# Kernel optimization log

Measured on AMD Instinct MI355X. Metric: run time of the kernel, lower is better.

## Reference

```python
import jax, jax.numpy as jnp
import numpy as np

N_NODES = 100000
N_USERS = 60000
N_MOVIES = 40000
N_EDGES = 1200000
D_IN = 64
D_EMB = 64


def setup_inputs() -> dict:
    key = jax.random.key(0)
    ks = jax.random.split(key, 6)
    x = jax.random.normal(ks[0], (N_NODES, D_IN), dtype=jnp.float32)
    edge_index = jax.random.randint(ks[1], (2, N_EDGES), 0, N_NODES, dtype=jnp.int64)
    # Glorot-ish init for the two GCNConv linear weights
    W1 = jax.random.normal(ks[2], (D_IN, D_EMB), dtype=jnp.float32) * (1.0 / np.sqrt(D_IN))
    b1 = jnp.zeros((D_EMB,), dtype=jnp.float32)
    W2 = jax.random.normal(ks[3], (D_EMB, D_EMB), dtype=jnp.float32) * (1.0 / np.sqrt(D_EMB))
    b2 = jnp.zeros((D_EMB,), dtype=jnp.float32)
    return {"x": x, "edge_index": edge_index, "W1": W1, "b1": b1, "W2": W2, "b2": b2}


def gcn_conv(x, W, b, src, dst):
    """PyG GCNConv: D^{-1/2}(A+I)D^{-1/2} X W + b with symmetric norm and self-loops."""
    h = x @ W  # [N, D_out]
    ones = jnp.ones(src.shape[0], dtype=h.dtype)
    # degree includes self-loop (+1)
    deg = jax.ops.segment_sum(ones, dst, num_segments=N_NODES) + 1.0
    dinv = jax.lax.rsqrt(deg)  # [N]
    coef = dinv[src] * dinv[dst]  # [E]
    agg = jax.ops.segment_sum(h[src] * coef[:, None], dst, num_segments=N_NODES)
    # self-loop contribution: norm = dinv[i]^2
    return agg + h * (dinv * dinv)[:, None] + b


def reference(x, edge_index, W1, b1, W2, b2):
    src, dst = edge_index[0], edge_index[1]
    h = gcn_conv(x, W1, b1, src, dst)
    h = jax.nn.relu(h)  # dropout is identity in eval mode
    h = gcn_conv(h, W2, b2, src, dst)
    user = h[:N_USERS]
    movie = h[N_USERS:N_USERS + N_MOVIES]
    return user, movie, h
```

## Files before the change

kernel.cpp:

```cpp
#include <hip/hip_runtime.h>

#define NN 100000
#define NE 1200000
#define DD 64
#define SCH 1024
#define SNB ((NN + SCH - 1) / SCH)

#define KCH3 96
#define CEH3 (NE / KCH3)
#define P3 4
#define BINS3 (NN / P3)
#define BINW3 (BINS3 / 4)
#define KSEG 4
#define KPS (KCH3 / KSEG)
#define NW4 (NN / 4)
#define HISTB (KCH3 * P3)
#define GEMMB ((NN + 255) / 256)

static __device__ __forceinline__ unsigned short f2bf(float f) {
    unsigned int u = __float_as_uint(f);
    u += 0x7fffu + ((u >> 16) & 1u);
    return (unsigned short)(u >> 16);
}
static __device__ __forceinline__ float bf_lo(unsigned int u) { return __uint_as_float(u << 16); }
static __device__ __forceinline__ float bf_hi(unsigned int u) { return __uint_as_float(u & 0xffff0000u); }

__global__ __launch_bounds__(1024) void k_histgemm(const int* __restrict__ dst,
                                                   unsigned char* __restrict__ H,
                                                   unsigned char* __restrict__ rank8,
                                                   const float* __restrict__ X,
                                                   const float* __restrict__ W,
                                                   unsigned short* __restrict__ Hb) {
    __shared__ union SM {
        unsigned int bins[BINW3];
        struct { float4 Ws4[64][16]; float Xs[64][68]; } g;
    } sm;
    int t = threadIdx.x;
    if (blockIdx.x < HISTB) {
        int k = blockIdx.x >> 2;
        int p = blockIdx.x & 3;
        for (int i = t; i < BINW3; i += 1024) sm.bins[i] = 0u;
        __syncthreads();
        int lo = p * BINS3;
        int beg = k * CEH3;
        for (int e4 = beg + t * 4; e4 < beg + CEH3; e4 += 4096) {
            int4 d4 = *(const int4*)&dst[e4];
            int dd[4] = {d4.x, d4.y, d4.z, d4.w};
#pragma unroll
            for (int j = 0; j < 4; ++j) {
                unsigned int r = (unsigned int)(dd[j] - lo);
                if (r < (unsigned int)BINS3) {
                    unsigned int sh = (r & 3u) << 3;
                    unsigned int old = atomicAdd(&sm.bins[r >> 2], 1u << sh);
                    rank8[e4 + j] = (unsigned char)((old >> sh) & 0xffu);
                }
            }
        }
        __syncthreads();
        unsigned int* Hw = (unsigned int*)(H + (size_t)k * NN + lo);
        for (int i = t; i < BINW3; i += 1024) Hw[i] = sm.bins[i];
    } else {
        const float4* W4 = (const float4*)W;
        sm.g.Ws4[t >> 4][t & 15] = W4[t];
        int row0 = (int)(blockIdx.x - HISTB) * 256;
        const float4* X4 = (const float4*)X;
        int r = t >> 4, q = t & 15;
#pragma unroll
        for (int s = 0; s < 4; ++s) {
            int row = row0 + s * 64 + r;
            float4 v = make_float4(0.f, 0.f, 0.f, 0.f);
            if (row < NN) v = X4[row * 16 + q];
            __syncthreads();
            *((float4*)&sm.g.Xs[r][q * 4]) = v;
            __syncthreads();
            float4 acc = make_float4(0.f, 0.f, 0.f, 0.f);
#pragma unroll 4
            for (int k = 0; k < 64; ++k) {
                float4 w = sm.g.Ws4[k][q];
                float x = sm.g.Xs[r][k];
                acc.x += x * w.x; acc.y += x * w.y; acc.z += x * w.z; acc.w += x * w.w;
            }
            if (row < NN) {
                ushort4 o;
                o.x = f2bf(acc.x); o.y = f2bf(acc.y); o.z = f2bf(acc.z); o.w = f2bf(acc.w);
                *((ushort4*)&Hb[(size_t)row * 64 + q * 4]) = o;
            }
        }
    }
}

__global__ __launch_bounds__(256) void k_cseg_sum(const unsigned int* __restrict__ H32,
                                                  unsigned int* __restrict__ aux) {
    int wd = blockIdx.x * 256 + threadIdx.x;
    int seg = blockIdx.y;
    if (wd >= NW4) return;
    unsigned int s = 0;
#pragma unroll
    for (int k = 0; k < KPS; ++k)
        s += H32[(size_t)(seg * KPS + k) * NW4 + wd];
    aux[seg * NW4 + wd] = s;
}

__global__ __launch_bounds__(256) void k_cseg_scan2(unsigned int* __restrict__ H32,
                                                    const unsigned int* __restrict__ aux,
                                                    int* __restrict__ rowptr,
                                                    int* __restrict__ part,
                                                    float* __restrict__ dinv) {
    __shared__ int wsum[4];
    int t = threadIdx.x;
    int wd = blockIdx.x * 256 + t;
    int seg = blockIdx.y;
    bool valid = wd < NW4;
    unsigned int s = 0;
    if (valid) {
        unsigned int base = 0;
        for (int i = 0; i < seg; ++i) base += aux[i * NW4 + wd];
        s = base;
#pragma unroll
        for (int k = 0; k < KPS; ++k) {
            size_t idx = (size_t)(seg * KPS + k) * NW4 + wd;
            unsigned int v = H32[idx];
            H32[idx] = s;
            s += v;
        }
    }
    if (seg != KSEG - 1) return;
    int d0 = valid ? (int)(s & 0xffu) : 0;
    int d1 = valid ? (int)((s >> 8) & 0xffu) : 0;
    int d2 = valid ? (int)((s >> 16) & 0xffu) : 0;
    int d3 = valid ? (int)(s >> 24) : 0;
    int idx = blockIdx.x * SCH + t * 4;
    if (valid) {
        float4 dv;
        dv.x = rsqrtf((float)d0 + 1.0f);
        dv.y = rsqrtf((float)d1 + 1.0f);
        dv.z = rsqrtf((float)d2 + 1.0f);
        dv.w = rsqrtf((float)d3 + 1.0f);
        *(float4*)&dinv[idx] = dv;
    }
    int ssum = d0 + d1 + d2 + d3;
    int lane = t & 63;
    int incl = ssum;
#pragma unroll
    for (int off = 1; off < 64; off <<= 1) {
        int v = __shfl_up(incl, off);
        if (lane >= off) incl += v;
    }
    int wv = t >> 6;
    if (lane == 63) wsum[wv] = incl;
    __syncthreads();
    int woff = 0;
#pragma unroll
    for (int i = 0; i < 4; ++i) if (i < wv) woff += wsum[i];
    int excl = woff + incl - ssum;
    if (valid) {
        int4 rp = make_int4(excl, excl + d0, excl + d0 + d1, excl + d0 + d1 + d2);
        *(int4*)&rowptr[idx] = rp;
    }
    if (t == 255) part[blockIdx.x] = woff + incl;
}

__global__ __launch_bounds__(128) void k_scan_part(int* __restrict__ part, int* __restrict__ rowptr) {
    __shared__ int sm[128];
    int t = threadIdx.x;
    int v = (t < SNB) ? part[t] : 0;
    sm[t] = v;
    __syncthreads();
    for (int off = 1; off < 128; off <<= 1) {
        int add = (t >= off) ? sm[t - off] : 0;
        __syncthreads();
        sm[t] += add;
        __syncthreads();
    }
    if (t == SNB - 1) rowptr[NN] = v;
    if (t < SNB) part[t] = sm[t] - v;
}

__global__ __launch_bounds__(256) void k_fill4(const int* __restrict__ src,
                                               const int* __restrict__ dst,
                                               const unsigned char* __restrict__ rank8,
                                               const unsigned char* __restrict__ H,
                                               const int* __restrict__ rowptr,
                                               const int* __restrict__ part,
                                               const float* __restrict__ dinv,
                                               int2* __restrict__ cc) {
    int e4 = (blockIdx.x * 256 + threadIdx.x) * 4;
    if (e4 >= NE) return;
    int4 d4 = *(const int4*)&dst[e4];
    int4 s4 = *(const int4*)&src[e4];
    unsigned int r4 = *(const unsigned int*)&rank8[e4];
    int dd[4] = {d4.x, d4.y, d4.z, d4.w};
    int ss[4] = {s4.x, s4.y, s4.z, s4.w};
    int k = e4 / CEH3;
#pragma unroll
    for (int j = 0; j < 4; ++j) {
        int d = dd[j], s = ss[j];
        int base = rowptr[d] + part[d >> 10] + (int)H[(size_t)k * NN + d];
        int pos = base + (int)((r4 >> (8 * j)) & 0xffu);
        cc[pos] = make_int2(s, __float_as_int(dinv[s] * dinv[d]));
    }
}

__global__ void k_hist_rank(const int* __restrict__ dst, int* __restrict__ degi,
                            int* __restrict__ rank, int ne) {
    int i = blockIdx.x * blockDim.x + threadIdx.x;
    if (i < ne) rank[i] = atomicAdd(&degi[dst[i]], 1);
}

__global__ __launch_bounds__(256) void k_scan_local(const int* __restrict__ degi,
                                                    int* __restrict__ rowptr,
                                                    int* __restrict__ part,
                                                    float* __restrict__ dinv) {
    __shared__ int wsum[4];
    int t = threadIdx.x;
    int idx = blockIdx.x * SCH + t * 4;
    int d0 = 0, d1 = 0, d2 = 0, d3 = 0;
    if (idx + 3 < NN) {
        int4 v = *(const int4*)&degi[idx];
        d0 = v.x; d1 = v.y; d2 = v.z; d3 = v.w;
        float4 dv;
        dv.x = rsqrtf((float)d0 + 1.0f);
        dv.y = rsqrtf((float)d1 + 1.0f);
        dv.z = rsqrtf((float)d2 + 1.0f);
        dv.w = rsqrtf((float)d3 + 1.0f);
        *(float4*)&dinv[idx] = dv;
    } else {
        if (idx     < NN) { d0 = degi[idx];     dinv[idx]     = rsqrtf((float)d0 + 1.0f); }
        if (idx + 1 < NN) { d1 = degi[idx + 1]; dinv[idx + 1] = rsqrtf((float)d1 + 1.0f); }
        if (idx + 2 < NN) { d2 = degi[idx + 2]; dinv[idx + 2] = rsqrtf((float)d2 + 1.0f); }
        if (idx + 3 < NN) { d3 = degi[idx + 3]; dinv[idx + 3] = rsqrtf((float)d3 + 1.0f); }
    }
    int s = d0 + d1 + d2 + d3;
    int lane = t & 63;
    int incl = s;
#pragma unroll
    for (int off = 1; off < 64; off <<= 1) {
        int v = __shfl_up(incl, off);
        if (lane >= off) incl += v;
    }
    int wv = t >> 6;
    if (lane == 63) wsum[wv] = incl;
    __syncthreads();
    int woff = 0;
#pragma unroll
    for (int i = 0; i < 4; ++i) if (i < wv) woff += wsum[i];
    int excl = woff + incl - s;
    if (idx     < NN) rowptr[idx]     = excl;
    if (idx + 1 < NN) rowptr[idx + 1] = excl + d0;
    if (idx + 2 < NN) rowptr[idx + 2] = excl + d0 + d1;
    if (idx + 3 < NN) rowptr[idx + 3] = excl + d0 + d1 + d2;
    if (t == 255) part[blockIdx.x] = woff + incl;
}

__global__ void k_scan_add(int* __restrict__ rowptr, const int* __restrict__ part) {
    int i = blockIdx.x * blockDim.x + threadIdx.x;
    if (i < NN) rowptr[i] += part[i >> 10];
    if (i == 0) rowptr[NN] = NE;
}

__global__ void k_fill_rank(const int* __restrict__ src, const int* __restrict__ dst,
                            const int* __restrict__ rank, const int* __restrict__ rowptr,
                            int* __restrict__ csr_src, int ne) {
    int e = blockIdx.x * blockDim.x + threadIdx.x;
    if (e < ne) csr_src[rowptr[dst[e]] + rank[e]] = src[e];
}

__global__ __launch_bounds__(256) void k_pack(const int* __restrict__ rowptr,
                                              const int* __restrict__ csr,
                                              const float* __restrict__ dinv,
                                              int2* __restrict__ cc) {
    int n = blockIdx.x * 256 + threadIdx.x;
    if (n >= NN) return;
    float dn = dinv[n];
    for (int e = rowptr[n]; e < rowptr[n + 1]; ++e) {
        int s = csr[e];
        cc[e] = make_int2(s, __float_as_int(dinv[s] * dn));
    }
}

__global__ __launch_bounds__(256) void k_gemm_bf(const float* __restrict__ X,
                                                 const float* __restrict__ W,
                                                 unsigned short* __restrict__ Hb,
                                                 int nrows) {
    __shared__ float4 Ws4[64][16];
    __shared__ float  Xs[64][68];
    int tid = threadIdx.x;
    const float4* W4 = (const float4*)W;
    for (int i = tid; i < 64 * 16; i += 256) Ws4[i >> 4][i & 15] = W4[i];
    int row0 = blockIdx.x * 64;
    const float4* X4 = (const float4*)X;
    for (int i = tid; i < 64 * 16; i += 256) {
        int r = i >> 4, q = i & 15;
        int row = row0 + r;
        float4 v = make_float4(0.f, 0.f, 0.f, 0.f);
        if (row < nrows) v = X4[row * 16 + q];
        *((float4*)&Xs[r][q * 4]) = v;
    }
    __syncthreads();
    int c4 = tid & 15;
    int rg = tid >> 4;
    float4 acc0 = make_float4(0.f, 0.f, 0.f, 0.f);
    float4 acc1 = acc0, acc2 = acc0, acc3 = acc0;
#pragma unroll 4
    for (int k = 0; k < 64; ++k) {
        float4 w = Ws4[k][c4];
        float x0 = Xs[rg * 4 + 0][k];
        float x1 = Xs[rg * 4 + 1][k];
        float x2 = Xs[rg * 4 + 2][k];
        float x3 = Xs[rg * 4 + 3][k];
        acc0.x += x0 * w.x; acc0.y += x0 * w.y; acc0.z += x0 * w.z; acc0.w += x0 * w.w;
        acc1.x += x1 * w.x; acc1.y += x1 * w.y; acc1.z += x1 * w.z; acc1.w += x1 * w.w;
        acc2.x += x2 * w.x; acc2.y += x2 * w.y; acc2.z += x2 * w.z; acc2.w += x2 * w.w;
        acc3.x += x3 * w.x; acc3.y += x3 * w.y; acc3.z += x3 * w.z; acc3.w += x3 * w.w;
    }
    float4 accs[4] = {acc0, acc1, acc2, acc3};
#pragma unroll
    for (int i = 0; i < 4; ++i) {
        int row = row0 + rg * 4 + i;
        if (row < nrows) {
            ushort4 o;
            o.x = f2bf(accs[i].x); o.y = f2bf(accs[i].y);
            o.z = f2bf(accs[i].z); o.w = f2bf(accs[i].w);
            *((ushort4*)&Hb[row * 64 + c4 * 4]) = o;
        }
    }
}

static __device__ __forceinline__ void gather8(const unsigned short* __restrict__ Hb,
                                               const int2* __restrict__ cc,
                                               int e0, int deg, int dmax, int cg,
                                               float acc[8]) {
#define LDE(T, S, C) { bool _v = (T) < deg; int2 _w = _v ? cc[e0 + (T)] : make_int2(0, 0); \
                       S = _w.x; C = __int_as_float(_w.y); }
#define GAT(U, S) U = *(const uint4*)(Hb + (size_t)(S) * 64 + cg * 8);
#define CONS(U, C) { acc[0] += bf_lo(U.x) * (C);  acc[1] += bf_hi(U.x) * (C); \
                     acc[2] += bf_lo(U.y) * (C);  acc[3] += bf_hi(U.y) * (C); \
                     acc[4] += bf_lo(U.z) * (C);  acc[5] += bf_hi(U.z) * (C); \
                     acc[6] += bf_lo(U.w) * (C);  acc[7] += bf_hi(U.w) * (C); }
    int s0, s1, s2, s3; float c0, c1, c2, c3;
    LDE(0, s0, c0); LDE(1, s1, c1); LDE(2, s2, c2); LDE(3, s3, c3);
    uint4 u0, u1, u2, u3;
    GAT(u0, s0); GAT(u1, s1); GAT(u2, s2); GAT(u3, s3);
    for (int t = 0; t < dmax; t += 4) {
        int sn0, sn1, sn2, sn3; float cn0, cn1, cn2, cn3;
        LDE(t + 4, sn0, cn0); LDE(t + 5, sn1, cn1);
        LDE(t + 6, sn2, cn2); LDE(t + 7, sn3, cn3);
        CONS(u0, c0); GAT(u0, sn0); c0 = cn0;
        CONS(u1, c1); GAT(u1, sn1); c1 = cn1;
        CONS(u2, c2); GAT(u2, sn2); c2 = cn2;
        CONS(u3, c3); GAT(u3, sn3); c3 = cn3;
    }
#undef LDE
#undef GAT
#undef CONS
}

__global__ __launch_bounds__(256) void k_reduce_g2(const unsigned short* __restrict__ Hb,
                                                   const int* __restrict__ rowptr,
                                                   const int* __restrict__ part,
                                                   const int2* __restrict__ cc,
                                                   const float* __restrict__ dinv,
                                                   const float* __restrict__ bias,
                                                   const float* __restrict__ W2,
                                                   unsigned short* __restrict__ Hb2) {
    __shared__ float4 Ws4[64][16];
    __shared__ float rows[32][68];
    int t = threadIdx.x;
    const float4* W4 = (const float4*)W2;
    for (int i = t; i < 1024; i += 256) Ws4[i >> 4][i & 15] = W4[i];

    int n = blockIdx.x * 32 + (t >> 3);
    int cg = t & 7;
    bool nv = n < NN;
    float din = nv ? dinv[n] : 0.f;
    uint4 us = make_uint4(0u, 0u, 0u, 0u);
    int e0 = 0, deg = 0;
    if (nv) {
        us = *(const uint4*)(Hb + (size_t)n * 64 + cg * 8);
        int rp0 = rowptr[n] + part[n >> 10];
        int rp1 = rowptr[n + 1] + part[(n + 1) >> 10];
        e0 = rp0; deg = rp1 - rp0;
    }
    int dmax = deg;
    dmax = max(dmax, __shfl_xor(dmax, 8));
    dmax = max(dmax, __shfl_xor(dmax, 16));
    dmax = max(dmax, __shfl_xor(dmax, 32));

    float acc[8];
#pragma unroll
    for (int j = 0; j < 8; ++j) acc[j] = 0.f;
    gather8(Hb, cc, e0, deg, dmax, cg, acc);

    float ddn = din * din;
    float4 b0 = *(const float4*)(bias + cg * 8);
    float4 b1 = *(const float4*)(bias + cg * 8 + 4);
    float4 o0, o1;
    o0.x = fmaxf(acc[0] + bf_lo(us.x) * ddn + b0.x, 0.f);
    o0.y = fmaxf(acc[1] + bf_hi(us.x) * ddn + b0.y, 0.f);
    o0.z = fmaxf(acc[2] + bf_lo(us.y) * ddn + b0.z, 0.f);
    o0.w = fmaxf(acc[3] + bf_hi(us.y) * ddn + b0.w, 0.f);
    o1.x = fmaxf(acc[4] + bf_lo(us.z) * ddn + b1.x, 0.f);
    o1.y = fmaxf(acc[5] + bf_hi(us.z) * ddn + b1.y, 0.f);
    o1.z = fmaxf(acc[6] + bf_lo(us.w) * ddn + b1.z, 0.f);
    o1.w = fmaxf(acc[7] + bf_hi(us.w) * ddn + b1.w, 0.f);
    int node = t >> 3;
    *(float4*)&rows[node][cg * 8]     = o0;
    *(float4*)&rows[node][cg * 8 + 4] = o1;
    __syncthreads();

    int c2 = t & 7;
    float a0 = 0.f, a1 = 0.f, a2 = 0.f, a3 = 0.f, a4 = 0.f, a5 = 0.f, a6 = 0.f, a7 = 0.f;
#pragma unroll 4
    for (int k = 0; k < 64; ++k) {
        float r = rows[node][k];
        float4 w0 = Ws4[k][c2 * 2];
        float4 w1 = Ws4[k][c2 * 2 + 1];
        a0 += r * w0.x; a1 += r * w0.y; a2 += r * w0.z; a3 += r * w0.w;
        a4 += r * w1.x; a5 += r * w1.y; a6 += r * w1.z; a7 += r * w1.w;
    }
    if (nv) {
        uint4 pk;
        pk.x = (unsigned int)f2bf(a0) | ((unsigned int)f2bf(a1) << 16);
        pk.y = (unsigned int)f2bf(a2) | ((unsigned int)f2bf(a3) << 16);
        pk.z = (unsigned int)f2bf(a4) | ((unsigned int)f2bf(a5) << 16);
        pk.w = (unsigned int)f2bf(a6) | ((unsigned int)f2bf(a7) << 16);
        *(uint4*)&Hb2[(size_t)n * 64 + c2 * 8] = pk;
    }
}

__global__ __launch_bounds__(256) void k_reduce2(const unsigned short* __restrict__ Hb,
                                                 const int* __restrict__ rowptr,
                                                 const int* __restrict__ part,
                                                 const int2* __restrict__ cc,
                                                 const float* __restrict__ dinv,
                                                 const float* __restrict__ bias,
                                                 float* __restrict__ out0,
                                                 float* __restrict__ out1) {
    int n = blockIdx.x * 32 + (threadIdx.x >> 3);
    if (n >= NN) return;
    int cg = threadIdx.x & 7;
    float din = dinv[n];
    uint4 us = *(const uint4*)(Hb + (size_t)n * 64 + cg * 8);
    int rp0 = rowptr[n] + part[n >> 10];
    int rp1 = rowptr[n + 1] + part[(n + 1) >> 10];
    int e0 = rp0, deg = rp1 - rp0;
    int dmax = deg;
    dmax = max(dmax, __shfl_xor(dmax, 8));
    dmax = max(dmax, __shfl_xor(dmax, 16));
    dmax = max(dmax, __shfl_xor(dmax, 32));

    float acc[8];
#pragma unroll
    for (int j = 0; j < 8; ++j) acc[j] = 0.f;
    gather8(Hb, cc, e0, deg, dmax, cg, acc);

    float ddn = din * din;
    float4 b0 = *(const float4*)(bias + cg * 8);
    float4 b1 = *(const float4*)(bias + cg * 8 + 4);
    float4 o0, o1;
    o0.x = acc[0] + bf_lo(us.x) * ddn + b0.x;
    o0.y = acc[1] + bf_hi(us.x) * ddn + b0.y;
    o0.z = acc[2] + bf_lo(us.y) * ddn + b0.z;
    o0.w = acc[3] + bf_hi(us.y) * ddn + b0.w;
    o1.x = acc[4] + bf_lo(us.z) * ddn + b1.x;
    o1.y = acc[5] + bf_hi(us.z) * ddn + b1.y;
    o1.z = acc[6] + bf_lo(us.w) * ddn + b1.z;
    o1.w = acc[7] + bf_hi(us.w) * ddn + b1.w;
    *(float4*)(out0 + (size_t)n * 64 + cg * 8)     = o0;
    *(float4*)(out0 + (size_t)n * 64 + cg * 8 + 4) = o1;
    *(float4*)(out1 + (size_t)n * 64 + cg * 8)     = o0;
    *(float4*)(out1 + (size_t)n * 64 + cg * 8 + 4) = o1;
}

extern "C" void kernel_launch(void* const* d_in, const int* in_sizes, int n_in,
                              void* d_out, int out_size, void* d_ws, size_t ws_size,
                              hipStream_t stream) {
    const float* x  = (const float*)d_in[0];
    const int*   ei = (const int*)d_in[1];
    const float* W1 = (const float*)d_in[2];
    const float* b1 = (const float*)d_in[3];
    const float* W2 = (const float*)d_in[4];
    const float* b2 = (const float*)d_in[5];
    const int* src = ei;
    const int* dst = ei + NE;

    float* A = (float*)d_out;
    float* B = (float*)d_out + (size_t)NN * DD;

    char* w = (char*)d_ws;
    size_t off = 0;
    auto alloc = [&](size_t bytes) { void* p = w + off; off += (bytes + 255) & ~(size_t)255; return p; };
    float* dinv   = (float*)alloc(NN * sizeof(float));
    int*   degi   = (int*)  alloc(NN * sizeof(int));
    int*   cnt    = (int*)  alloc(NN * sizeof(int));
    int*   rowptr = (int*)  alloc((NN + 1) * sizeof(int));
    int*   part   = (int*)  alloc(512 * sizeof(int));
    int*   csr    = (int*)  alloc(NE * sizeof(int));
    int2*  cc     = (int2*) alloc(NE * sizeof(int2));
    void*  uni    = alloc((size_t)NN * DD * sizeof(unsigned short));
    unsigned char* Hh    = (unsigned char*)uni;
    unsigned char* rank8 = (unsigned char*)uni + (size_t)KCH3 * NN;
    unsigned short* Bb2  = (unsigned short*)uni;
    unsigned short* Bb1 = (unsigned short*)alloc((size_t)NN * DD * sizeof(unsigned short));
    int* rank = (int*)Bb1;
    size_t off_total = off;

    bool new_path = (ws_size >= off_total);

    if (new_path) {
        k_histgemm<<<HISTB + GEMMB, 1024, 0, stream>>>(dst, Hh, rank8, x, W1, Bb1);
        dim3 cgrid((NW4 + 255) / 256, KSEG);
        k_cseg_sum<<<cgrid, 256, 0, stream>>>((unsigned int*)Hh, (unsigned int*)cnt);
        k_cseg_scan2<<<cgrid, 256, 0, stream>>>((unsigned int*)Hh, (const unsigned int*)cnt,
                                                rowptr, part, dinv);
        k_scan_part<<<1, 128, 0, stream>>>(part, rowptr);
        k_fill4<<<(NE / 4 + 255) / 256, 256, 0, stream>>>(src, dst, rank8, Hh, rowptr, part, dinv, cc);
        k_reduce_g2<<<(NN + 31) / 32, 256, 0, stream>>>(Bb1, rowptr, part, cc, dinv, b1, W2, Bb2);
        k_reduce2<<<(NN + 31) / 32, 256, 0, stream>>>(Bb2, rowptr, part, cc, dinv, b2, A, B);
    } else {
        hipMemsetAsync(degi, 0, NN * sizeof(int), stream);
        k_hist_rank<<<(NE + 255) / 256, 256, 0, stream>>>(dst, degi, rank, NE);
        k_scan_local<<<SNB, 256, 0, stream>>>(degi, rowptr, part, dinv);
        k_scan_part<<<1, 128, 0, stream>>>(part, rowptr);
        k_scan_add<<<(NN + 255) / 256, 256, 0, stream>>>(rowptr, part);
        hipMemsetAsync(part, 0, 512 * sizeof(int), stream);
        k_fill_rank<<<(NE + 255) / 256, 256, 0, stream>>>(src, dst, rank, rowptr, csr, NE);
        k_pack<<<(NN + 255) / 256, 256, 0, stream>>>(rowptr, csr, dinv, cc);
        k_gemm_bf<<<(NN + 63) / 64, 256, 0, stream>>>(x, W1, Bb1, NN);
        k_reduce_g2<<<(NN + 31) / 32, 256, 0, stream>>>(Bb1, rowptr, part, cc, dinv, b1, W2, Bb2);
        k_reduce2<<<(NN + 31) / 32, 256, 0, stream>>>(Bb2, rowptr, part, cc, dinv, b2, A, B);
    }
}
```

Measured before the change: 231.8 us.

## Merge segmented column scan into one kernel and halve histogram partitions

Replaces the two-pass segmented scan over the 96 per-chunk byte histograms (sum kernel plus scan kernel over 4 segments) with a single kernel that scans all 96 chunks serially per word, removing one launch and the auxiliary buffer. The histogram phase now splits nodes into 2 partitions instead of 4, so shared-memory bins double and fewer blocks each read the dst array. Bounds checks in the reduce kernels are dropped because NN divides evenly by 32. The trade-off is less parallelism in the scan (a 96-long serial chain per thread over fewer blocks) and larger LDS usage per histogram block, which may lower occupancy.

```diff
diff --git a/kernel.cpp b/kernel.cpp
--- a/kernel.cpp
+++ b/kernel.cpp
@@ -8,11 +8,9 @@
 
 #define KCH3 96
 #define CEH3 (NE / KCH3)
-#define P3 4
+#define P3 2
 #define BINS3 (NN / P3)
 #define BINW3 (BINS3 / 4)
-#define KSEG 4
-#define KPS (KCH3 / KSEG)
 #define NW4 (NN / 4)
 #define HISTB (KCH3 * P3)
 #define GEMMB ((NN + 255) / 256)
@@ -37,8 +35,8 @@
     } sm;
     int t = threadIdx.x;
     if (blockIdx.x < HISTB) {
-        int k = blockIdx.x >> 2;
-        int p = blockIdx.x & 3;
+        int k = blockIdx.x >> 1;
+        int p = blockIdx.x & 1;
         for (int i = t; i < BINW3; i += 1024) sm.bins[i] = 0u;
         __syncthreads();
         int lo = p * BINS3;
@@ -89,42 +87,24 @@
     }
 }
 
-__global__ __launch_bounds__(256) void k_cseg_sum(const unsigned int* __restrict__ H32,
-                                                  unsigned int* __restrict__ aux) {
-    int wd = blockIdx.x * 256 + threadIdx.x;
-    int seg = blockIdx.y;
-    if (wd >= NW4) return;
-    unsigned int s = 0;
-#pragma unroll
-    for (int k = 0; k < KPS; ++k)
-        s += H32[(size_t)(seg * KPS + k) * NW4 + wd];
-    aux[seg * NW4 + wd] = s;
-}
-
-__global__ __launch_bounds__(256) void k_cseg_scan2(unsigned int* __restrict__ H32,
-                                                    const unsigned int* __restrict__ aux,
-                                                    int* __restrict__ rowptr,
-                                                    int* __restrict__ part,
-                                                    float* __restrict__ dinv) {
+__global__ __launch_bounds__(256) void k_cseg(unsigned int* __restrict__ H32,
+                                              int* __restrict__ rowptr,
+                                              int* __restrict__ part,
+                                              float* __restrict__ dinv) {
     __shared__ int wsum[4];
     int t = threadIdx.x;
     int wd = blockIdx.x * 256 + t;
-    int seg = blockIdx.y;
     bool valid = wd < NW4;
     unsigned int s = 0;
     if (valid) {
-        unsigned int base = 0;
-        for (int i = 0; i < seg; ++i) base += aux[i * NW4 + wd];
-        s = base;
-#pragma unroll
-        for (int k = 0; k < KPS; ++k) {
-            size_t idx = (size_t)(seg * KPS + k) * NW4 + wd;
+#pragma unroll 8
+        for (int k = 0; k < KCH3; ++k) {
+            size_t idx = (size_t)k * NW4 + wd;
             unsigned int v = H32[idx];
             H32[idx] = s;
             s += v;
         }
     }
-    if (seg != KSEG - 1) return;
     int d0 = valid ? (int)(s & 0xffu) : 0;
     int d1 = valid ? (int)((s >> 8) & 0xffu) : 0;
     int d2 = valid ? (int)((s >> 16) & 0xffu) : 0;
@@ -371,16 +351,11 @@
 
     int n = blockIdx.x * 32 + (t >> 3);
     int cg = t & 7;
-    bool nv = n < NN;
-    float din = nv ? dinv[n] : 0.f;
-    uint4 us = make_uint4(0u, 0u, 0u, 0u);
-    int e0 = 0, deg = 0;
-    if (nv) {
-        us = *(const uint4*)(Hb + (size_t)n * 64 + cg * 8);
-        int rp0 = rowptr[n] + part[n >> 10];
-        int rp1 = rowptr[n + 1] + part[(n + 1) >> 10];
-        e0 = rp0; deg = rp1 - rp0;
-    }
+    float din = dinv[n];
+    uint4 us = *(const uint4*)(Hb + (size_t)n * 64 + cg * 8);
+    int rp0 = rowptr[n] + part[n >> 10];
+    int rp1 = rowptr[n + 1] + part[(n + 1) >> 10];
+    int e0 = rp0, deg = rp1 - rp0;
     int dmax = deg;
     dmax = max(dmax, __shfl_xor(dmax, 8));
     dmax = max(dmax, __shfl_xor(dmax, 16));
@@ -418,14 +393,12 @@
         a0 += r * w0.x; a1 += r * w0.y; a2 += r * w0.z; a3 += r * w0.w;
         a4 += r * w1.x; a5 += r * w1.y; a6 += r * w1.z; a7 += r * w1.w;
     }
-    if (nv) {
-        uint4 pk;
-        pk.x = (unsigned int)f2bf(a0) | ((unsigned int)f2bf(a1) << 16);
-        pk.y = (unsigned int)f2bf(a2) | ((unsigned int)f2bf(a3) << 16);
-        pk.z = (unsigned int)f2bf(a4) | ((unsigned int)f2bf(a5) << 16);
-        pk.w = (unsigned int)f2bf(a6) | ((unsigned int)f2bf(a7) << 16);
-        *(uint4*)&Hb2[(size_t)n * 64 + c2 * 8] = pk;
-    }
+    uint4 pk;
+    pk.x = (unsigned int)f2bf(a0) | ((unsigned int)f2bf(a1) << 16);
+    pk.y = (unsigned int)f2bf(a2) | ((unsigned int)f2bf(a3) << 16);
+    pk.z = (unsigned int)f2bf(a4) | ((unsigned int)f2bf(a5) << 16);
+    pk.w = (unsigned int)f2bf(a6) | ((unsigned int)f2bf(a7) << 16);
+    *(uint4*)&Hb2[(size_t)n * 64 + c2 * 8] = pk;
 }
 
 __global__ __launch_bounds__(256) void k_reduce2(const unsigned short* __restrict__ Hb,
@@ -437,7 +410,6 @@
                                                  float* __restrict__ out0,
                                                  float* __restrict__ out1) {
     int n = blockIdx.x * 32 + (threadIdx.x >> 3);
-    if (n >= NN) return;
     int cg = threadIdx.x & 7;
     float din = dinv[n];
     uint4 us = *(const uint4*)(Hb + (size_t)n * 64 + cg * 8);
@@ -509,14 +481,11 @@
 
     if (new_path) {
         k_histgemm<<<HISTB + GEMMB, 1024, 0, stream>>>(dst, Hh, rank8, x, W1, Bb1);
-        dim3 cgrid((NW4 + 255) / 256, KSEG);
-        k_cseg_sum<<<cgrid, 256, 0, stream>>>((unsigned int*)Hh, (unsigned int*)cnt);
-        k_cseg_scan2<<<cgrid, 256, 0, stream>>>((unsigned int*)Hh, (const unsigned int*)cnt,
-                                                rowptr, part, dinv);
+        k_cseg<<<(NW4 + 255) / 256, 256, 0, stream>>>((unsigned int*)Hh, rowptr, part, dinv);
         k_scan_part<<<1, 128, 0, stream>>>(part, rowptr);
         k_fill4<<<(NE / 4 + 255) / 256, 256, 0, stream>>>(src, dst, rank8, Hh, rowptr, part, dinv, cc);
-        k_reduce_g2<<<(NN + 31) / 32, 256, 0, stream>>>(Bb1, rowptr, part, cc, dinv, b1, W2, Bb2);
-        k_reduce2<<<(NN + 31) / 32, 256, 0, stream>>>(Bb2, rowptr, part, cc, dinv, b2, A, B);
+        k_reduce_g2<<<NN / 32, 256, 0, stream>>>(Bb1, rowptr, part, cc, dinv, b1, W2, Bb2);
+        k_reduce2<<<NN / 32, 256, 0, stream>>>(Bb2, rowptr, part, cc, dinv, b2, A, B);
     } else {
         hipMemsetAsync(degi, 0, NN * sizeof(int), stream);
         k_hist_rank<<<(NE + 255) / 256, 256, 0, stream>>>(dst, degi, rank, NE);
@@ -527,7 +496,7 @@
         k_fill_rank<<<(NE + 255) / 256, 256, 0, stream>>>(src, dst, rank, rowptr, csr, NE);
         k_pack<<<(NN + 255) / 256, 256, 0, stream>>>(rowptr, csr, dinv, cc);
         k_gemm_bf<<<(NN + 63) / 64, 256, 0, stream>>>(x, W1, Bb1, NN);
-        k_reduce_g2<<<(NN + 31) / 32, 256, 0, stream>>>(Bb1, rowptr, part, cc, dinv, b1, W2, Bb2);
-        k_reduce2<<<(NN + 31) / 32, 256, 0, stream>>>(Bb2, rowptr, part, cc, dinv, b2, A, B);
-    }
-}
+        k_reduce_g2<<<NN / 32, 256, 0, stream>>>(Bb1, rowptr, part, cc, dinv, b1, W2, Bb2);
+        k_reduce2<<<NN / 32, 256, 0, stream>>>(Bb2, rowptr, part, cc, dinv, b2, A, B);
+    }
+}
```

After: 230.9 us. No clear change (-0.4%).
